# Optimization experiments

Measured on AMD Instinct MI355X. Metric: run time of the kernel, lower is better.

## Reference

```python
import jax, jax.numpy as jnp
import numpy as np

B, T, D, H = 256, 512, 128, 128  # batch, seq_len, input feat, hidden


def setup_inputs() -> dict:
    key = jax.random.key(0)
    ks = jax.random.split(key, 7)
    s_in = 1.0 / np.sqrt(D)
    s_h = 1.0 / np.sqrt(H)
    return {
        "x": jax.random.normal(ks[0], (B, T, D), dtype=jnp.float32),
        # layer 0: kernel [D, 3H], recurrent kernel [H, 3H], bias [2, 3H] (reset_after=True)
        "W0": jax.random.uniform(ks[1], (D, 3 * H), jnp.float32, -s_in, s_in),
        "U0": jax.random.uniform(ks[2], (H, 3 * H), jnp.float32, -s_h, s_h),
        "b0": jnp.zeros((2, 3 * H), jnp.float32),
        # layer 1: input dim = H
        "W1": jax.random.uniform(ks[3], (H, 3 * H), jnp.float32, -s_h, s_h),
        "U1": jax.random.uniform(ks[4], (H, 3 * H), jnp.float32, -s_h, s_h),
        "b1": jnp.zeros((2, 3 * H), jnp.float32),
    }


def _gru_layer(x, W, U, b):
    """Keras GRU (reset_after=True), return_sequences=True, eval mode (no dropout).
    x: [B, T, D]; W: [D, 3H]; U: [H, 3H]; b: [2, 3H]. Gate order: z, r, h.
    """
    b_in, b_rec = b[0], b[1]
    # precompute input projection for all timesteps: [B, T, 3H]
    xp = jnp.einsum("btd,dg->btg", x, W) + b_in
    h0 = jnp.zeros((x.shape[0], U.shape[0]), x.dtype)

    def step(h, xt):
        rec = h @ U + b_rec                       # [B, 3H]
        xz, xr, xh = jnp.split(xt, 3, axis=-1)
        rz, rr, rh = jnp.split(rec, 3, axis=-1)
        z = jax.nn.sigmoid(xz + rz)
        r = jax.nn.sigmoid(xr + rr)
        hh = jnp.tanh(xh + r * rh)                # reset applied after recurrent matmul
        h_new = z * h + (1.0 - z) * hh
        return h_new, h_new

    _, ys = jax.lax.scan(step, h0, jnp.swapaxes(xp, 0, 1))  # [T, B, H]
    return jnp.swapaxes(ys, 0, 1)                            # [B, T, H]


def reference(x, W0, U0, b0, W1, U1, b1):
    h = _gru_layer(x, W0, U0, b0)
    h = _gru_layer(h, W1, U1, b1)
    return h
```

## Files before the change

kernel.cpp:

```cpp
#include <hip/hip_runtime.h>
#include <cstdint>
#include <cstddef>

typedef __bf16 bf16x8 __attribute__((ext_vector_type(8)));
typedef __bf16 bf16x4 __attribute__((ext_vector_type(4)));
typedef float  f32x4  __attribute__((ext_vector_type(4)));

#define MFMA16(a,b,c) __builtin_amdgcn_mfma_f32_16x16x32_bf16((a),(b),(c),0,0,0)

#define BAR_LGKM() __asm__ volatile("s_waitcnt lgkmcnt(0)\n\ts_barrier" ::: "memory")
#define BAR_FULL() __asm__ volatile("s_waitcnt vmcnt(0) lgkmcnt(0)\n\ts_barrier" ::: "memory")

#define L2E  1.4426950408889634f
#define L2E2 2.8853900817779268f


__global__ void prep_frags(const float* __restrict__ W0, const float* __restrict__ U0,
                           const float* __restrict__ W1, const float* __restrict__ U1,
                           __bf16* __restrict__ frags, int* __restrict__ flags)
{
    if (blockIdx.x == 0 && threadIdx.x < 16) flags[threadIdx.x * 16] = 0;
    int id = blockIdx.x * 512 + threadIdx.x;
    int layer = id / 12288;
    int r     = id % 12288;
    int lane = r & 63;
    int ctkt = r >> 6;
    int kt = ctkt & 7;
    int ct = ctkt >> 3;
    const float* Wsrc = layer ? W1 : W0;
    const float* Usrc = layer ? U1 : U0;
    int n  = ct * 16 + (lane & 15);
    int k0 = kt * 32 + (lane >> 4) * 8;
    const float* src = (k0 < 128) ? (Wsrc + (size_t)k0 * 384)
                                  : (Usrc + (size_t)(k0 - 128) * 384);
    const float s = (ct < 16) ? L2E : L2E2;
    __bf16* dst = frags + (size_t)layer * 98304 + (size_t)r * 8;
#pragma unroll
    for (int j = 0; j < 8; j++)
        dst[j] = (__bf16)(src[(size_t)j * 384 + n] * s);
}

__global__ __launch_bounds__(512, 2) void gru_pipe(
    const float* x, const __bf16* __restrict__ frags,
    const float* __restrict__ b0, const float* __restrict__ b1,
    float* h0, float* out, int* flags)
{
    __shared__ __align__(16) __bf16 xb[2][2048];
    __shared__ __align__(16) __bf16 hb[2][2048];

    const int tid  = threadIdx.x;
    const int wave = tid >> 6, lane = tid & 63;
    const int l15  = lane & 15, quad = lane >> 4;
    const int pair  = blockIdx.x & 15;
    const int layer = blockIdx.x >> 4;
    const int B0 = pair * 16;
    int* const flagp = flags + pair * 16;

    const __bf16* Bf  = frags + (size_t)layer * 98304;
    const float* bias = layer ? b1 : b0;
    const float* xin  = layer ? h0 : x;
    float*       hout = layer ? out : h0;

    bf16x8 bw[3][4], bu[3][4];
#pragma unroll
    for (int g = 0; g < 3; g++) {
        int ct = 8 * g + wave;
#pragma unroll
        for (int kt = 0; kt < 4; kt++) {
            bw[g][kt] = *(const bf16x8*)(Bf + (size_t)((ct * 8 + kt) * 64 + lane) * 8);
            bu[g][kt] = *(const bf16x8*)(Bf + (size_t)((ct * 8 + kt + 4) * 64 + lane) * 8);
            __asm__ volatile("" : "+v"(bw[g][kt]));
            __asm__ volatile("" : "+v"(bu[g][kt]));
        }
    }

    const int j = wave * 16 + l15;
    const float bz  = (bias[j]       + bias[384 + j]) * L2E;
    const float br  = (bias[128 + j] + bias[512 + j]) * L2E;
    const float bxh = bias[256 + j] * L2E2;
    const float brh = bias[640 + j] * L2E2;

    const int srow = tid >> 5;
    const float* px = xin + (size_t)(B0 + srow) * 65536 + (tid & 31) * 4;
    const int sb = (srow * 256 + (tid & 31) * 8) ^ ((srow & 7) << 4);

    const int swz = (l15 & 7) << 4;
    const int abb = l15 * 256 + quad * 16;
    const int ao0 = (abb      ) ^ swz;
    const int ao1 = (abb +  64) ^ swz;
    const int ao2 = (abb + 128) ^ swz;
    const int ao3 = (abb + 192) ^ swz;
    int hw_[4];
#pragma unroll
    for (int r = 0; r < 4; r++) {
        int row = quad * 4 + r;
        hw_[r] = (row * 256 + j * 2) ^ ((row & 7) << 4);
    }

    const size_t obase = (size_t)(B0 + quad * 4) * 65536 + j;

    int known = 0;
    if (layer) {
        while (known < 4) {
            __builtin_amdgcn_s_sleep(4);
            known = __hip_atomic_load(flagp, __ATOMIC_RELAXED,
                                      __HIP_MEMORY_SCOPE_AGENT);
        }
    }

#define LOADX(p) (layer ? __builtin_nontemporal_load((const f32x4*)(p)) \
                        : *(const f32x4*)(p))
#define PACKST(buf, v) do { bf16x4 hv_;                                  \
        hv_.x = (__bf16)(v)[0]; hv_.y = (__bf16)(v)[1];                  \
        hv_.z = (__bf16)(v)[2]; hv_.w = (__bf16)(v)[3];                  \
        *(bf16x4*)((char*)&(buf)[0] + sb) = hv_; } while (0)

    const f32x4 zv = {0.f, 0.f, 0.f, 0.f};

    {
        f32x4 v0 = LOADX(px);
        f32x4 v1 = LOADX(px + 128);
        PACKST(xb[0], v0);
        PACKST(xb[1], v1);
        ((uint64_t*)&hb[0][0])[tid] = 0ull;
    }
    __syncthreads();

    f32x4 xpzE = zv, xprE = zv, xphE = zv;
    f32x4 xpzO = zv, xprO = zv, xphO = zv;
    {
        bf16x8 Ax0 = *(const bf16x8*)((const char*)&xb[0][0] + ao0);
        bf16x8 Ax1 = *(const bf16x8*)((const char*)&xb[0][0] + ao1);
        bf16x8 Ax2 = *(const bf16x8*)((const char*)&xb[0][0] + ao2);
        bf16x8 Ax3 = *(const bf16x8*)((const char*)&xb[0][0] + ao3);
        xpzE = MFMA16(Ax0, bw[0][0], xpzE); xprE = MFMA16(Ax0, bw[1][0], xprE); xphE = MFMA16(Ax0, bw[2][0], xphE);
        xpzE = MFMA16(Ax1, bw[0][1], xpzE); xprE = MFMA16(Ax1, bw[1][1], xprE); xphE = MFMA16(Ax1, bw[2][1], xphE);
        xpzE = MFMA16(Ax2, bw[0][2], xpzE); xprE = MFMA16(Ax2, bw[1][2], xprE); xphE = MFMA16(Ax2, bw[2][2], xphE);
        xpzE = MFMA16(Ax3, bw[0][3], xpzE); xprE = MFMA16(Ax3, bw[1][3], xprE); xphE = MFMA16(Ax3, bw[2][3], xphE);
    }
    {
        bf16x8 Ax0 = *(const bf16x8*)((const char*)&xb[1][0] + ao0);
        bf16x8 Ax1 = *(const bf16x8*)((const char*)&xb[1][0] + ao1);
        bf16x8 Ax2 = *(const bf16x8*)((const char*)&xb[1][0] + ao2);
        bf16x8 Ax3 = *(const bf16x8*)((const char*)&xb[1][0] + ao3);
        xpzO = MFMA16(Ax0, bw[0][0], xpzO); xprO = MFMA16(Ax0, bw[1][0], xprO); xphO = MFMA16(Ax0, bw[2][0], xphO);
        xpzO = MFMA16(Ax1, bw[0][1], xpzO); xprO = MFMA16(Ax1, bw[1][1], xprO); xphO = MFMA16(Ax1, bw[2][1], xphO);
        xpzO = MFMA16(Ax2, bw[0][2], xpzO); xprO = MFMA16(Ax2, bw[1][2], xprO); xphO = MFMA16(Ax2, bw[2][2], xphO);
        xpzO = MFMA16(Ax3, bw[0][3], xpzO); xprO = MFMA16(Ax3, bw[1][3], xprO); xphO = MFMA16(Ax3, bw[2][3], xphO);
    }
    __syncthreads();
    {
        f32x4 v2 = LOADX(px + 256);
        PACKST(xb[0], v2);
    }
    f32x4 vc = LOADX(px + 384);
    float hold[4] = {0.f, 0.f, 0.f, 0.f};
    __syncthreads();

#define GRU_BODY(T, S, xpz, xpr, xph)                                         \
    {                                                                         \
        const int t_ = (T);                                                   \
        if (layer) {                                  \
            int need = t_ + 5; if (need > 512) need = 512;                    \
            while (known < need) {                                            \
                __builtin_amdgcn_s_sleep(4);                                  \
                known = __hip_atomic_load(flagp, __ATOMIC_RELAXED,            \
                                          __HIP_MEMORY_SCOPE_AGENT);          \
            }                                                                 \
        }                                                                     \
        int t4_ = t_ + 4; if (t4_ > 511) t4_ = 511;                           \
        f32x4 vn = LOADX(px + (size_t)t4_ * 128);                             \
        bf16x8 Ah0 = *(const bf16x8*)((const char*)&hb[S][0] + ao0);          \
        bf16x8 Ah1 = *(const bf16x8*)((const char*)&hb[S][0] + ao1);          \
        bf16x8 Ah2 = *(const bf16x8*)((const char*)&hb[S][0] + ao2);          \
        bf16x8 Ah3 = *(const bf16x8*)((const char*)&hb[S][0] + ao3);          \
        f32x4 az = xpz, ar = xpr, ahh = zv;                                   \
        __builtin_amdgcn_s_setprio(1);                                        \
        az = MFMA16(Ah0, bu[0][0], az); ar = MFMA16(Ah0, bu[1][0], ar);       \
        ahh = MFMA16(Ah0, bu[2][0], ahh);                                     \
        az = MFMA16(Ah1, bu[0][1], az); ar = MFMA16(Ah1, bu[1][1], ar);       \
        ahh = MFMA16(Ah1, bu[2][1], ahh);                                     \
        az = MFMA16(Ah2, bu[0][2], az); ar = MFMA16(Ah2, bu[1][2], ar);       \
        ahh = MFMA16(Ah2, bu[2][2], ahh);                                     \
        az = MFMA16(Ah3, bu[0][3], az); ar = MFMA16(Ah3, bu[1][3], ar);       \
        ahh = MFMA16(Ah3, bu[2][3], ahh);                                     \
            \
        bf16x8 Ax0 = *(const bf16x8*)((const char*)&xb[S][0] + ao0);          \
        bf16x8 Ax1 = *(const bf16x8*)((const char*)&xb[S][0] + ao1);          \
        bf16x8 Ax2 = *(const bf16x8*)((const char*)&xb[S][0] + ao2);          \
        bf16x8 Ax3 = *(const bf16x8*)((const char*)&xb[S][0] + ao3);          \
        f32x4 xhc = xph;                             \
        xpz = zv; xpr = zv; xph = zv;                                         \
        xpz = MFMA16(Ax0, bw[0][0], xpz); xpr = MFMA16(Ax0, bw[1][0], xpr);   \
        xph = MFMA16(Ax0, bw[2][0], xph);                                     \
        xpz = MFMA16(Ax1, bw[0][1], xpz); xpr = MFMA16(Ax1, bw[1][1], xpr);   \
        xph = MFMA16(Ax1, bw[2][1], xph);                                     \
        xpz = MFMA16(Ax2, bw[0][2], xpz); xpr = MFMA16(Ax2, bw[1][2], xpr);   \
        xph = MFMA16(Ax2, bw[2][2], xph);                                     \
        xpz = MFMA16(Ax3, bw[0][3], xpz); xpr = MFMA16(Ax3, bw[1][3], xpr);   \
        xph = MFMA16(Ax3, bw[2][3], xph);                                     \
        __builtin_amdgcn_s_setprio(0);                                        \
                        \
        float hnew[4];                                                        \
        _Pragma("unroll")                                                     \
        for (int r = 0; r < 4; r++) {                                         \
            float z  = __builtin_amdgcn_rcpf(                                 \
                           1.f + __builtin_amdgcn_exp2f(-(az[r] + bz)));      \
            float rg = __builtin_amdgcn_rcpf(                                 \
                           1.f + __builtin_amdgcn_exp2f(-(ar[r] + br)));      \
            float hp = (xhc[r] + bxh) + rg * (ahh[r] + brh);                  \
            float e2 = __builtin_amdgcn_exp2f(hp);                            \
            float th = 1.f - 2.f * __builtin_amdgcn_rcpf(e2 + 1.f);           \
            hnew[r] = th + z * (hold[r] - th);                                \
            hold[r] = hnew[r];                                                \
        }                                                                     \
                         \
        PACKST(xb[(S) ^ 1], vc);                                              \
        _Pragma("unroll")                                                     \
        for (int r = 0; r < 4; r++)                                           \
            *(__bf16*)((char*)&hb[(S) ^ 1][0] + hw_[r]) = (__bf16)hnew[r];    \
        if (layer == 0 && (t_ & 3) == 3) {                                    \
            BAR_FULL();                 \
            if (tid == 0)                                                     \
                __hip_atomic_store(flagp, t_, __ATOMIC_RELAXED,               \
                                   __HIP_MEMORY_SCOPE_AGENT);                 \
        } else {                                                              \
            BAR_LGKM();                                                       \
        }                                                                     \
        if (layer == 0) {                                                     \
            _Pragma("unroll")                                                 \
            for (int r = 0; r < 4; r++)                                       \
                __builtin_nontemporal_store(hnew[r],                          \
                    hout + obase + (size_t)r * 65536 + (size_t)t_ * 128);     \
        } else {                                                              \
            _Pragma("unroll")                                                 \
            for (int r = 0; r < 4; r++)                                       \
                hout[obase + (size_t)r * 65536 + (size_t)t_ * 128] = hnew[r]; \
        }                                                                     \
        vc = vn;                                                              \
    }

    for (int it = 0; it < 256; ++it) {
        GRU_BODY(2 * it,     0, xpzE, xprE, xphE);
        GRU_BODY(2 * it + 1, 1, xpzO, xprO, xphO);
    }
#undef GRU_BODY
#undef PACKST
#undef LOADX

    if (layer == 0) {
        BAR_FULL();
        if (tid == 0)
            __hip_atomic_store(flagp, 512, __ATOMIC_RELAXED,
                               __HIP_MEMORY_SCOPE_AGENT);
    }
}

extern "C" void kernel_launch(void* const* d_in, const int* in_sizes, int n_in,
                              void* d_out, int out_size, void* d_ws, size_t ws_size,
                              hipStream_t stream)
{
    const float* x  = (const float*)d_in[0];
    const float* W0 = (const float*)d_in[1];
    const float* U0 = (const float*)d_in[2];
    const float* b0 = (const float*)d_in[3];
    const float* W1 = (const float*)d_in[4];
    const float* U1 = (const float*)d_in[5];
    const float* b1 = (const float*)d_in[6];
    float* out = (float*)d_out;

    char* ws = (char*)d_ws;
    __bf16* frags = (__bf16*)ws;
    int*    flags = (int*)(ws + 393216);
    float* h0;
    const size_t need = 458752 + 67108864;
    if (ws_size >= need) h0 = (float*)(ws + 458752);
    else                 h0 = out;

    prep_frags<<<48, 512, 0, stream>>>(W0, U0, W1, U1, frags, flags);
    gru_pipe<<<32, 512, 0, stream>>>(x, frags, b0, b1, h0, out, flags);
}
```

Measured before the change: 552.5 us.

## Stagger MFMA order across waves and poll layer flags every four steps

Splits waves into two groups. Even waves issue the recurrent MFMAs before the input-projection MFMAs, and odd waves issue them in the reverse order, so the waves sharing a SIMD contend less for the matrix unit at the same moment. The layer-1 dependency poll now runs only every fourth step with an eight-step lookahead instead of every step, cutting atomic loads and sleeps. The larger lag raises layer-1 startup latency and adds branch divergence between the two code variants.

```diff
diff --git a/kernel.cpp b/kernel.cpp
--- a/kernel.cpp
+++ b/kernel.cpp
@@ -101,7 +101,7 @@
 
     int known = 0;
     if (layer) {
-        while (known < 4) {
+        while (known < 8) {
             __builtin_amdgcn_s_sleep(4);
             known = __hip_atomic_load(flagp, __ATOMIC_RELAXED,
                                       __HIP_MEMORY_SCOPE_AGENT);
@@ -157,69 +157,35 @@
     float hold[4] = {0.f, 0.f, 0.f, 0.f};
     __syncthreads();
 
-#define GRU_BODY(T, S, xpz, xpr, xph)                                         \
-    {                                                                         \
-        const int t_ = (T);                                                   \
-        if (layer) {                                  \
-            int need = t_ + 5; if (need > 512) need = 512;                    \
+#define POLL4(t_)                                                             \
+        if (layer && (((t_) & 3) == 0)) {                                     \
+            int need = (t_) + 8; if (need > 512) need = 512;                   \
             while (known < need) {                                            \
                 __builtin_amdgcn_s_sleep(4);                                  \
                 known = __hip_atomic_load(flagp, __ATOMIC_RELAXED,            \
                                           __HIP_MEMORY_SCOPE_AGENT);          \
             }                                                                 \
-        }                                                                     \
-        int t4_ = t_ + 4; if (t4_ > 511) t4_ = 511;                           \
-        f32x4 vn = LOADX(px + (size_t)t4_ * 128);                             \
-        bf16x8 Ah0 = *(const bf16x8*)((const char*)&hb[S][0] + ao0);          \
-        bf16x8 Ah1 = *(const bf16x8*)((const char*)&hb[S][0] + ao1);          \
-        bf16x8 Ah2 = *(const bf16x8*)((const char*)&hb[S][0] + ao2);          \
-        bf16x8 Ah3 = *(const bf16x8*)((const char*)&hb[S][0] + ao3);          \
-        f32x4 az = xpz, ar = xpr, ahh = zv;                                   \
-        __builtin_amdgcn_s_setprio(1);                                        \
-        az = MFMA16(Ah0, bu[0][0], az); ar = MFMA16(Ah0, bu[1][0], ar);       \
-        ahh = MFMA16(Ah0, bu[2][0], ahh);                                     \
-        az = MFMA16(Ah1, bu[0][1], az); ar = MFMA16(Ah1, bu[1][1], ar);       \
-        ahh = MFMA16(Ah1, bu[2][1], ahh);                                     \
-        az = MFMA16(Ah2, bu[0][2], az); ar = MFMA16(Ah2, bu[1][2], ar);       \
-        ahh = MFMA16(Ah2, bu[2][2], ahh);                                     \
-        az = MFMA16(Ah3, bu[0][3], az); ar = MFMA16(Ah3, bu[1][3], ar);       \
-        ahh = MFMA16(Ah3, bu[2][3], ahh);                                     \
-            \
-        bf16x8 Ax0 = *(const bf16x8*)((const char*)&xb[S][0] + ao0);          \
-        bf16x8 Ax1 = *(const bf16x8*)((const char*)&xb[S][0] + ao1);          \
-        bf16x8 Ax2 = *(const bf16x8*)((const char*)&xb[S][0] + ao2);          \
-        bf16x8 Ax3 = *(const bf16x8*)((const char*)&xb[S][0] + ao3);          \
-        f32x4 xhc = xph;                             \
-        xpz = zv; xpr = zv; xph = zv;                                         \
-        xpz = MFMA16(Ax0, bw[0][0], xpz); xpr = MFMA16(Ax0, bw[1][0], xpr);   \
-        xph = MFMA16(Ax0, bw[2][0], xph);                                     \
-        xpz = MFMA16(Ax1, bw[0][1], xpz); xpr = MFMA16(Ax1, bw[1][1], xpr);   \
-        xph = MFMA16(Ax1, bw[2][1], xph);                                     \
-        xpz = MFMA16(Ax2, bw[0][2], xpz); xpr = MFMA16(Ax2, bw[1][2], xpr);   \
-        xph = MFMA16(Ax2, bw[2][2], xph);                                     \
-        xpz = MFMA16(Ax3, bw[0][3], xpz); xpr = MFMA16(Ax3, bw[1][3], xpr);   \
-        xph = MFMA16(Ax3, bw[2][3], xph);                                     \
-        __builtin_amdgcn_s_setprio(0);                                        \
-                        \
+        }
+
+#define GRU_TAIL(t_, S, azv, arv, xhcv, ahhv)                                 \
         float hnew[4];                                                        \
         _Pragma("unroll")                                                     \
         for (int r = 0; r < 4; r++) {                                         \
             float z  = __builtin_amdgcn_rcpf(                                 \
-                           1.f + __builtin_amdgcn_exp2f(-(az[r] + bz)));      \
+                           1.f + __builtin_amdgcn_exp2f(-((azv)[r] + bz)));   \
             float rg = __builtin_amdgcn_rcpf(                                 \
-                           1.f + __builtin_amdgcn_exp2f(-(ar[r] + br)));      \
-            float hp = (xhc[r] + bxh) + rg * (ahh[r] + brh);                  \
+                           1.f + __builtin_amdgcn_exp2f(-((arv)[r] + br)));   \
+            float hp = ((xhcv)[r] + bxh) + rg * ((ahhv)[r] + brh);            \
             float e2 = __builtin_amdgcn_exp2f(hp);                            \
             float th = 1.f - 2.f * __builtin_amdgcn_rcpf(e2 + 1.f);           \
             hnew[r] = th + z * (hold[r] - th);                                \
             hold[r] = hnew[r];                                                \
         }                                                                     \
-                         \
         PACKST(xb[(S) ^ 1], vc);                                              \
         _Pragma("unroll")                                                     \
         for (int r = 0; r < 4; r++)                                           \
             *(__bf16*)((char*)&hb[(S) ^ 1][0] + hw_[r]) = (__bf16)hnew[r];    \
-        if (layer == 0 && (t_ & 3) == 3) {                                    \
+        if (layer == 0 && ((t_) & 3) == 3) {                                  \
             BAR_FULL();                 \
             if (tid == 0)                                                     \
                 __hip_atomic_store(flagp, t_, __ATOMIC_RELAXED,               \
@@ -237,14 +203,98 @@
             for (int r = 0; r < 4; r++)                                       \
                 hout[obase + (size_t)r * 65536 + (size_t)t_ * 128] = hnew[r]; \
         }                                                                     \
-        vc = vn;                                                              \
-    }
-
-    for (int it = 0; it < 256; ++it) {
-        GRU_BODY(2 * it,     0, xpzE, xprE, xphE);
-        GRU_BODY(2 * it + 1, 1, xpzO, xprO, xphO);
-    }
-#undef GRU_BODY
+        vc = vn;
+
+#define GRU_RF(T, S, xpz, xpr, xph)                                           \
+    {                                                                         \
+        const int t_ = (T);                                                   \
+        POLL4(t_);                                                            \
+        int t4_ = t_ + 4; if (t4_ > 511) t4_ = 511;                           \
+        f32x4 vn = LOADX(px + (size_t)t4_ * 128);                             \
+        bf16x8 Ah0 = *(const bf16x8*)((const char*)&hb[S][0] + ao0);          \
+        bf16x8 Ah1 = *(const bf16x8*)((const char*)&hb[S][0] + ao1);          \
+        bf16x8 Ah2 = *(const bf16x8*)((const char*)&hb[S][0] + ao2);          \
+        bf16x8 Ah3 = *(const bf16x8*)((const char*)&hb[S][0] + ao3);          \
+        __builtin_amdgcn_s_setprio(1);                                        \
+        f32x4 az  = MFMA16(Ah0, bu[0][0], xpz);                               \
+        f32x4 ar  = MFMA16(Ah0, bu[1][0], xpr);                               \
+        f32x4 ahh = MFMA16(Ah0, bu[2][0], zv);                                \
+        az = MFMA16(Ah1, bu[0][1], az); ar = MFMA16(Ah1, bu[1][1], ar);       \
+        ahh = MFMA16(Ah1, bu[2][1], ahh);                                     \
+        az = MFMA16(Ah2, bu[0][2], az); ar = MFMA16(Ah2, bu[1][2], ar);       \
+        ahh = MFMA16(Ah2, bu[2][2], ahh);                                     \
+        az = MFMA16(Ah3, bu[0][3], az); ar = MFMA16(Ah3, bu[1][3], ar);       \
+        ahh = MFMA16(Ah3, bu[2][3], ahh);                                     \
+        bf16x8 Ax0 = *(const bf16x8*)((const char*)&xb[S][0] + ao0);          \
+        bf16x8 Ax1 = *(const bf16x8*)((const char*)&xb[S][0] + ao1);          \
+        bf16x8 Ax2 = *(const bf16x8*)((const char*)&xb[S][0] + ao2);          \
+        bf16x8 Ax3 = *(const bf16x8*)((const char*)&xb[S][0] + ao3);          \
+        f32x4 xhc = xph;                             \
+        xpz = MFMA16(Ax0, bw[0][0], zv);  xpr = MFMA16(Ax0, bw[1][0], zv);    \
+        xph = MFMA16(Ax0, bw[2][0], zv);                                      \
+        xpz = MFMA16(Ax1, bw[0][1], xpz); xpr = MFMA16(Ax1, bw[1][1], xpr);   \
+        xph = MFMA16(Ax1, bw[2][1], xph);                                     \
+        xpz = MFMA16(Ax2, bw[0][2], xpz); xpr = MFMA16(Ax2, bw[1][2], xpr);   \
+        xph = MFMA16(Ax2, bw[2][2], xph);                                     \
+        xpz = MFMA16(Ax3, bw[0][3], xpz); xpr = MFMA16(Ax3, bw[1][3], xpr);   \
+        xph = MFMA16(Ax3, bw[2][3], xph);                                     \
+        __builtin_amdgcn_s_setprio(0);                                        \
+        GRU_TAIL(t_, S, az, ar, xhc, ahh)                                     \
+    }
+
+#define GRU_XF(T, S, xpz, xpr, xph)                                           \
+    {                                                                         \
+        const int t_ = (T);                                                   \
+        POLL4(t_);                                                            \
+        int t4_ = t_ + 4; if (t4_ > 511) t4_ = 511;                           \
+        f32x4 vn = LOADX(px + (size_t)t4_ * 128);                             \
+        bf16x8 Ax0 = *(const bf16x8*)((const char*)&xb[S][0] + ao0);          \
+        bf16x8 Ax1 = *(const bf16x8*)((const char*)&xb[S][0] + ao1);          \
+        bf16x8 Ax2 = *(const bf16x8*)((const char*)&xb[S][0] + ao2);          \
+        bf16x8 Ax3 = *(const bf16x8*)((const char*)&xb[S][0] + ao3);          \
+        __builtin_amdgcn_s_setprio(1);                                        \
+        f32x4 tz = MFMA16(Ax0, bw[0][0], zv);                                 \
+        f32x4 tr = MFMA16(Ax0, bw[1][0], zv);                                 \
+        f32x4 th2 = MFMA16(Ax0, bw[2][0], zv);                                \
+        tz = MFMA16(Ax1, bw[0][1], tz); tr = MFMA16(Ax1, bw[1][1], tr);       \
+        th2 = MFMA16(Ax1, bw[2][1], th2);                                     \
+        tz = MFMA16(Ax2, bw[0][2], tz); tr = MFMA16(Ax2, bw[1][2], tr);       \
+        th2 = MFMA16(Ax2, bw[2][2], th2);                                     \
+        tz = MFMA16(Ax3, bw[0][3], tz); tr = MFMA16(Ax3, bw[1][3], tr);       \
+        th2 = MFMA16(Ax3, bw[2][3], th2);                                     \
+        bf16x8 Ah0 = *(const bf16x8*)((const char*)&hb[S][0] + ao0);          \
+        bf16x8 Ah1 = *(const bf16x8*)((const char*)&hb[S][0] + ao1);          \
+        bf16x8 Ah2 = *(const bf16x8*)((const char*)&hb[S][0] + ao2);          \
+        bf16x8 Ah3 = *(const bf16x8*)((const char*)&hb[S][0] + ao3);          \
+        f32x4 az  = MFMA16(Ah0, bu[0][0], xpz);                               \
+        f32x4 ar  = MFMA16(Ah0, bu[1][0], xpr);                               \
+        f32x4 ahh = MFMA16(Ah0, bu[2][0], zv);                                \
+        az = MFMA16(Ah1, bu[0][1], az); ar = MFMA16(Ah1, bu[1][1], ar);       \
+        ahh = MFMA16(Ah1, bu[2][1], ahh);                                     \
+        az = MFMA16(Ah2, bu[0][2], az); ar = MFMA16(Ah2, bu[1][2], ar);       \
+        ahh = MFMA16(Ah2, bu[2][2], ahh);                                     \
+        az = MFMA16(Ah3, bu[0][3], az); ar = MFMA16(Ah3, bu[1][3], ar);       \
+        ahh = MFMA16(Ah3, bu[2][3], ahh);                                     \
+        __builtin_amdgcn_s_setprio(0);                                        \
+        GRU_TAIL(t_, S, az, ar, xph, ahh)                                     \
+        xpz = tz; xpr = tr; xph = th2;                                        \
+    }
+
+    if ((wave & 1) == 0) {
+        for (int it = 0; it < 256; ++it) {
+            GRU_RF(2 * it,     0, xpzE, xprE, xphE);
+            GRU_RF(2 * it + 1, 1, xpzO, xprO, xphO);
+        }
+    } else {
+        for (int it = 0; it < 256; ++it) {
+            GRU_XF(2 * it,     0, xpzE, xprE, xphE);
+            GRU_XF(2 * it + 1, 1, xpzO, xprO, xphO);
+        }
+    }
+#undef GRU_RF
+#undef GRU_XF
+#undef GRU_TAIL
+#undef POLL4
 #undef PACKST
 #undef LOADX
 
```

Result: slower. 590.1 us (+6.8%).

## Split batch across 256 blocks with 2 rows each instead of 16

Applied to the files above, without the earlier changes.

Each block now handles 2 batch rows instead of 16, so 128 layer pairs run as 256 blocks rather than 32, spreading the serial recurrence over many more CUs. The 16-row MFMA tile is padded, with only lanes for valid rows writing state and output, and only the first wave loads inputs. The layer-1 consumer polls the layer-0 flag with acquire/release ordering. This wastes most of each MFMA on padding but cuts per-step latency per CU, and raises occupancy and the number of flag pairs.

```diff
diff --git a/kernel.cpp b/kernel.cpp
--- a/kernel.cpp
+++ b/kernel.cpp
@@ -19,7 +19,7 @@
                            const float* __restrict__ W1, const float* __restrict__ U1,
                            __bf16* __restrict__ frags, int* __restrict__ flags)
 {
-    if (blockIdx.x == 0 && threadIdx.x < 16) flags[threadIdx.x * 16] = 0;
+    if (blockIdx.x == 0 && threadIdx.x < 128) flags[threadIdx.x * 16] = 0;
     int id = blockIdx.x * 512 + threadIdx.x;
     int layer = id / 12288;
     int r     = id % 12288;
@@ -45,15 +45,16 @@
     const float* __restrict__ b0, const float* __restrict__ b1,
     float* h0, float* out, int* flags)
 {
-    __shared__ __align__(16) __bf16 xb[2][2048];
-    __shared__ __align__(16) __bf16 hb[2][2048];
+    __shared__ __align__(16) __bf16 xb[2][256];
+    __shared__ __align__(16) __bf16 hb[2][256];
 
     const int tid  = threadIdx.x;
     const int wave = tid >> 6, lane = tid & 63;
     const int l15  = lane & 15, quad = lane >> 4;
-    const int pair  = blockIdx.x & 15;
-    const int layer = blockIdx.x >> 4;
-    const int B0 = pair * 16;
+    const int bid   = blockIdx.x;
+    const int layer = (bid >> 3) & 1;
+    const int pair  = (bid & 7) | ((bid >> 4) << 3);
+    const int B0 = pair * 2;
     int* const flagp = flags + pair * 16;
 
     const __bf16* Bf  = frags + (size_t)layer * 98304;
@@ -80,33 +81,17 @@
     const float bxh = bias[256 + j] * L2E2;
     const float brh = bias[640 + j] * L2E2;
 
-    const int srow = tid >> 5;
-    const float* px = xin + (size_t)(B0 + srow) * 65536 + (tid & 31) * 4;
-    const int sb = (srow * 256 + (tid & 31) * 8) ^ ((srow & 7) << 4);
-
-    const int swz = (l15 & 7) << 4;
-    const int abb = l15 * 256 + quad * 16;
-    const int ao0 = (abb      ) ^ swz;
-    const int ao1 = (abb +  64) ^ swz;
-    const int ao2 = (abb + 128) ^ swz;
-    const int ao3 = (abb + 192) ^ swz;
-    int hw_[4];
-#pragma unroll
-    for (int r = 0; r < 4; r++) {
-        int row = quad * 4 + r;
-        hw_[r] = (row * 256 + j * 2) ^ ((row & 7) << 4);
-    }
-
-    const size_t obase = (size_t)(B0 + quad * 4) * 65536 + j;
+    const int aoff = (l15 >> 3) * 256 + quad * 16;
+
+    const int  hwb = (quad >> 1) * 256 + j * 2;
+    const bool orow_ok = (quad & 1) == 0;
+    const size_t obase = (size_t)(B0 + (quad >> 1)) * 65536 + j;
+
+    const int sr = (tid >> 5) & 1;
+    const float* px = xin + (size_t)(B0 + sr) * 65536 + (tid & 31) * 4;
+    const int sb = sr * 256 + (tid & 31) * 8;
 
     int known = 0;
-    if (layer) {
-        while (known < 4) {
-            __builtin_amdgcn_s_sleep(4);
-            known = __hip_atomic_load(flagp, __ATOMIC_RELAXED,
-                                      __HIP_MEMORY_SCOPE_AGENT);
-        }
-    }
 
 #define LOADX(p) (layer ? __builtin_nontemporal_load((const f32x4*)(p)) \
                         : *(const f32x4*)(p))
@@ -114,10 +99,18 @@
         hv_.x = (__bf16)(v)[0]; hv_.y = (__bf16)(v)[1];                  \
         hv_.z = (__bf16)(v)[2]; hv_.w = (__bf16)(v)[3];                  \
         *(bf16x4*)((char*)&(buf)[0] + sb) = hv_; } while (0)
+#define POLL_ACQ(need_) do {                                             \
+        while (known < (need_)) {                                        \
+            __builtin_amdgcn_s_sleep(4);                                 \
+            known = __hip_atomic_load(flagp, __ATOMIC_ACQUIRE,           \
+                                      __HIP_MEMORY_SCOPE_AGENT);         \
+        } } while (0)
 
     const f32x4 zv = {0.f, 0.f, 0.f, 0.f};
-
-    {
+    f32x4 vc = zv;
+
+    if (tid < 64) {
+        if (layer) POLL_ACQ(4);
         f32x4 v0 = LOADX(px);
         f32x4 v1 = LOADX(px + 128);
         PACKST(xb[0], v0);
@@ -129,70 +122,68 @@
     f32x4 xpzE = zv, xprE = zv, xphE = zv;
     f32x4 xpzO = zv, xprO = zv, xphO = zv;
     {
-        bf16x8 Ax0 = *(const bf16x8*)((const char*)&xb[0][0] + ao0);
-        bf16x8 Ax1 = *(const bf16x8*)((const char*)&xb[0][0] + ao1);
-        bf16x8 Ax2 = *(const bf16x8*)((const char*)&xb[0][0] + ao2);
-        bf16x8 Ax3 = *(const bf16x8*)((const char*)&xb[0][0] + ao3);
+        bf16x8 Ax0 = *(const bf16x8*)((const char*)&xb[0][0] + aoff);
+        bf16x8 Ax1 = *(const bf16x8*)((const char*)&xb[0][0] + aoff + 64);
+        bf16x8 Ax2 = *(const bf16x8*)((const char*)&xb[0][0] + aoff + 128);
+        bf16x8 Ax3 = *(const bf16x8*)((const char*)&xb[0][0] + aoff + 192);
         xpzE = MFMA16(Ax0, bw[0][0], xpzE); xprE = MFMA16(Ax0, bw[1][0], xprE); xphE = MFMA16(Ax0, bw[2][0], xphE);
         xpzE = MFMA16(Ax1, bw[0][1], xpzE); xprE = MFMA16(Ax1, bw[1][1], xprE); xphE = MFMA16(Ax1, bw[2][1], xphE);
         xpzE = MFMA16(Ax2, bw[0][2], xpzE); xprE = MFMA16(Ax2, bw[1][2], xprE); xphE = MFMA16(Ax2, bw[2][2], xphE);
         xpzE = MFMA16(Ax3, bw[0][3], xpzE); xprE = MFMA16(Ax3, bw[1][3], xprE); xphE = MFMA16(Ax3, bw[2][3], xphE);
     }
     {
-        bf16x8 Ax0 = *(const bf16x8*)((const char*)&xb[1][0] + ao0);
-        bf16x8 Ax1 = *(const bf16x8*)((const char*)&xb[1][0] + ao1);
-        bf16x8 Ax2 = *(const bf16x8*)((const char*)&xb[1][0] + ao2);
-        bf16x8 Ax3 = *(const bf16x8*)((const char*)&xb[1][0] + ao3);
+        bf16x8 Ax0 = *(const bf16x8*)((const char*)&xb[1][0] + aoff);
+        bf16x8 Ax1 = *(const bf16x8*)((const char*)&xb[1][0] + aoff + 64);
+        bf16x8 Ax2 = *(const bf16x8*)((const char*)&xb[1][0] + aoff + 128);
+        bf16x8 Ax3 = *(const bf16x8*)((const char*)&xb[1][0] + aoff + 192);
         xpzO = MFMA16(Ax0, bw[0][0], xpzO); xprO = MFMA16(Ax0, bw[1][0], xprO); xphO = MFMA16(Ax0, bw[2][0], xphO);
         xpzO = MFMA16(Ax1, bw[0][1], xpzO); xprO = MFMA16(Ax1, bw[1][1], xprO); xphO = MFMA16(Ax1, bw[2][1], xphO);
         xpzO = MFMA16(Ax2, bw[0][2], xpzO); xprO = MFMA16(Ax2, bw[1][2], xprO); xphO = MFMA16(Ax2, bw[2][2], xphO);
         xpzO = MFMA16(Ax3, bw[0][3], xpzO); xprO = MFMA16(Ax3, bw[1][3], xprO); xphO = MFMA16(Ax3, bw[2][3], xphO);
     }
     __syncthreads();
-    {
+    if (tid < 64) {
         f32x4 v2 = LOADX(px + 256);
         PACKST(xb[0], v2);
-    }
-    f32x4 vc = LOADX(px + 384);
-    float hold[4] = {0.f, 0.f, 0.f, 0.f};
+        vc = LOADX(px + 384);
+    }
+    float hold0 = 0.f;
     __syncthreads();
 
 #define GRU_BODY(T, S, xpz, xpr, xph)                                         \
     {                                                                         \
         const int t_ = (T);                                                   \
-        if (layer) {                                  \
-            int need = t_ + 5; if (need > 512) need = 512;                    \
-            while (known < need) {                                            \
-                __builtin_amdgcn_s_sleep(4);                                  \
-                known = __hip_atomic_load(flagp, __ATOMIC_RELAXED,            \
-                                          __HIP_MEMORY_SCOPE_AGENT);          \
+        f32x4 vn = zv;                                                        \
+        if (tid < 64) {                                                       \
+            if (layer) {                              \
+                int need = t_ + 5; if (need > 512) need = 512;                \
+                POLL_ACQ(need);                                               \
             }                                                                 \
+            int t4_ = t_ + 4; if (t4_ > 511) t4_ = 511;                       \
+            vn = LOADX(px + (size_t)t4_ * 128);                               \
         }                                                                     \
-        int t4_ = t_ + 4; if (t4_ > 511) t4_ = 511;                           \
-        f32x4 vn = LOADX(px + (size_t)t4_ * 128);                             \
-        bf16x8 Ah0 = *(const bf16x8*)((const char*)&hb[S][0] + ao0);          \
-        bf16x8 Ah1 = *(const bf16x8*)((const char*)&hb[S][0] + ao1);          \
-        bf16x8 Ah2 = *(const bf16x8*)((const char*)&hb[S][0] + ao2);          \
-        bf16x8 Ah3 = *(const bf16x8*)((const char*)&hb[S][0] + ao3);          \
-        f32x4 az = xpz, ar = xpr, ahh = zv;                                   \
+        bf16x8 Ah0 = *(const bf16x8*)((const char*)&hb[S][0] + aoff);         \
+        bf16x8 Ah1 = *(const bf16x8*)((const char*)&hb[S][0] + aoff + 64);    \
+        bf16x8 Ah2 = *(const bf16x8*)((const char*)&hb[S][0] + aoff + 128);   \
+        bf16x8 Ah3 = *(const bf16x8*)((const char*)&hb[S][0] + aoff + 192);   \
         __builtin_amdgcn_s_setprio(1);                                        \
-        az = MFMA16(Ah0, bu[0][0], az); ar = MFMA16(Ah0, bu[1][0], ar);       \
-        ahh = MFMA16(Ah0, bu[2][0], ahh);                                     \
+        f32x4 az  = MFMA16(Ah0, bu[0][0], xpz);                               \
+        f32x4 ar  = MFMA16(Ah0, bu[1][0], xpr);                               \
+        f32x4 ahh = MFMA16(Ah0, bu[2][0], zv);                                \
         az = MFMA16(Ah1, bu[0][1], az); ar = MFMA16(Ah1, bu[1][1], ar);       \
         ahh = MFMA16(Ah1, bu[2][1], ahh);                                     \
         az = MFMA16(Ah2, bu[0][2], az); ar = MFMA16(Ah2, bu[1][2], ar);       \
         ahh = MFMA16(Ah2, bu[2][2], ahh);                                     \
         az = MFMA16(Ah3, bu[0][3], az); ar = MFMA16(Ah3, bu[1][3], ar);       \
         ahh = MFMA16(Ah3, bu[2][3], ahh);                                     \
-            \
-        bf16x8 Ax0 = *(const bf16x8*)((const char*)&xb[S][0] + ao0);          \
-        bf16x8 Ax1 = *(const bf16x8*)((const char*)&xb[S][0] + ao1);          \
-        bf16x8 Ax2 = *(const bf16x8*)((const char*)&xb[S][0] + ao2);          \
-        bf16x8 Ax3 = *(const bf16x8*)((const char*)&xb[S][0] + ao3);          \
+        bf16x8 Ax0 = *(const bf16x8*)((const char*)&xb[S][0] + aoff);         \
+        bf16x8 Ax1 = *(const bf16x8*)((const char*)&xb[S][0] + aoff + 64);    \
+        bf16x8 Ax2 = *(const bf16x8*)((const char*)&xb[S][0] + aoff + 128);   \
+        bf16x8 Ax3 = *(const bf16x8*)((const char*)&xb[S][0] + aoff + 192);   \
         f32x4 xhc = xph;                             \
-        xpz = zv; xpr = zv; xph = zv;                                         \
-        xpz = MFMA16(Ax0, bw[0][0], xpz); xpr = MFMA16(Ax0, bw[1][0], xpr);   \
-        xph = MFMA16(Ax0, bw[2][0], xph);                                     \
+        xpz = MFMA16(Ax0, bw[0][0], zv);                                      \
+        xpr = MFMA16(Ax0, bw[1][0], zv);                                      \
+        xph = MFMA16(Ax0, bw[2][0], zv);                                      \
         xpz = MFMA16(Ax1, bw[0][1], xpz); xpr = MFMA16(Ax1, bw[1][1], xpr);   \
         xph = MFMA16(Ax1, bw[2][1], xph);                                     \
         xpz = MFMA16(Ax2, bw[0][2], xpz); xpr = MFMA16(Ax2, bw[1][2], xpr);   \
@@ -200,42 +191,33 @@
         xpz = MFMA16(Ax3, bw[0][3], xpz); xpr = MFMA16(Ax3, bw[1][3], xpr);   \
         xph = MFMA16(Ax3, bw[2][3], xph);                                     \
         __builtin_amdgcn_s_setprio(0);                                        \
-                        \
-        float hnew[4];                                                        \
-        _Pragma("unroll")                                                     \
-        for (int r = 0; r < 4; r++) {                                         \
-            float z  = __builtin_amdgcn_rcpf(                                 \
-                           1.f + __builtin_amdgcn_exp2f(-(az[r] + bz)));      \
-            float rg = __builtin_amdgcn_rcpf(                                 \
-                           1.f + __builtin_amdgcn_exp2f(-(ar[r] + br)));      \
-            float hp = (xhc[r] + bxh) + rg * (ahh[r] + brh);                  \
-            float e2 = __builtin_amdgcn_exp2f(hp);                            \
-            float th = 1.f - 2.f * __builtin_amdgcn_rcpf(e2 + 1.f);           \
-            hnew[r] = th + z * (hold[r] - th);                                \
-            hold[r] = hnew[r];                                                \
-        }                                                                     \
-                         \
-        PACKST(xb[(S) ^ 1], vc);                                              \
-        _Pragma("unroll")                                                     \
-        for (int r = 0; r < 4; r++)                                           \
-            *(__bf16*)((char*)&hb[(S) ^ 1][0] + hw_[r]) = (__bf16)hnew[r];    \
+                       \
+        float z  = __builtin_amdgcn_rcpf(                                     \
+                       1.f + __builtin_amdgcn_exp2f(-(az[0] + bz)));          \
+        float rg = __builtin_amdgcn_rcpf(                                     \
+                       1.f + __builtin_amdgcn_exp2f(-(ar[0] + br)));          \
+        float hp = (xhc[0] + bxh) + rg * (ahh[0] + brh);                      \
+        float e2 = __builtin_amdgcn_exp2f(hp);                                \
+        float th = 1.f - 2.f * __builtin_amdgcn_rcpf(e2 + 1.f);               \
+        float hn = th + z * (hold0 - th);                                     \
+        hold0 = hn;                                                           \
+        if (tid < 64) PACKST(xb[(S) ^ 1], vc);             \
+        if (orow_ok)                                                          \
+            *(__bf16*)((char*)&hb[(S) ^ 1][0] + hwb) = (__bf16)hn;            \
         if (layer == 0 && (t_ & 3) == 3) {                                    \
             BAR_FULL();                 \
             if (tid == 0)                                                     \
-                __hip_atomic_store(flagp, t_, __ATOMIC_RELAXED,               \
+                __hip_atomic_store(flagp, t_, __ATOMIC_RELEASE,               \
                                    __HIP_MEMORY_SCOPE_AGENT);                 \
         } else {                                                              \
             BAR_LGKM();                                                       \
         }                                                                     \
-        if (layer == 0) {                                                     \
-            _Pragma("unroll")                                                 \
-            for (int r = 0; r < 4; r++)                                       \
-                __builtin_nontemporal_store(hnew[r],                          \
-                    hout + obase + (size_t)r * 65536 + (size_t)t_ * 128);     \
-        } else {                                                              \
-            _Pragma("unroll")                                                 \
-            for (int r = 0; r < 4; r++)                                       \
-                hout[obase + (size_t)r * 65536 + (size_t)t_ * 128] = hnew[r]; \
+        if (orow_ok) {                                                        \
+            if (layer == 0)                                                   \
+                __builtin_nontemporal_store(hn,                               \
+                    hout + obase + (size_t)t_ * 128);                         \
+            else                                                              \
+                hout[obase + (size_t)t_ * 128] = hn;                          \
         }                                                                     \
         vc = vn;                                                              \
     }
@@ -245,13 +227,14 @@
         GRU_BODY(2 * it + 1, 1, xpzO, xprO, xphO);
     }
 #undef GRU_BODY
+#undef POLL_ACQ
 #undef PACKST
 #undef LOADX
 
     if (layer == 0) {
         BAR_FULL();
         if (tid == 0)
-            __hip_atomic_store(flagp, 512, __ATOMIC_RELAXED,
+            __hip_atomic_store(flagp, 512, __ATOMIC_RELEASE,
                                __HIP_MEMORY_SCOPE_AGENT);
     }
 }
@@ -278,5 +261,5 @@
     else                 h0 = out;
 
     prep_frags<<<48, 512, 0, stream>>>(W0, U0, W1, U1, frags, flags);
-    gru_pipe<<<32, 512, 0, stream>>>(x, frags, b0, b1, h0, out, flags);
+    gru_pipe<<<256, 512, 0, stream>>>(x, frags, b0, b1, h0, out, flags);
 }
```

New measurement: 799.8 us. 1.45x slower.
